# Optimization experiments

Measured on AMD Instinct MI355X. Metric: run time of the kernel, lower is better.

The kernel has to match this reference:

```python
import jax, jax.numpy as jnp
import numpy as np

D = 768

def _linear_params(key, name_idx, d_in, d_out):
    k1, k2 = jax.random.split(jax.random.fold_in(jax.random.key(42), name_idx))
    bound = 1.0 / np.sqrt(d_in)
    W = jax.random.uniform(k1, (d_out, d_in), jnp.float32, -bound, bound)
    b = jax.random.uniform(k2, (d_out,), jnp.float32, -bound, bound)
    return W, b

def setup_inputs() -> dict:
    key = jax.random.key(0)
    kq, kk, kv = jax.random.split(key, 3)
    B, S = 8, 2048
    inp = {
        'query': jax.random.normal(kq, (B, S, D), jnp.float32),
        'key': jax.random.normal(kk, (B, S, D), jnp.float32),
        'value': jax.random.normal(kv, (B, S, D), jnp.float32),
    }
    Wq, bq = _linear_params(key, 0, D, D)
    Wk, bk = _linear_params(key, 1, D, D)
    Wv, bv = _linear_params(key, 2, D, D)
    Wg1, bg1 = _linear_params(key, 3, D, D)
    Wg2, bg2 = _linear_params(key, 4, D, D)
    inp.update(Wq=Wq, bq=bq, Wk=Wk, bk=bk, Wv=Wv, bv=bv,
               Wg1=Wg1, bg1=bg1, Wg2=Wg2, bg2=bg2,
               text_scale=jnp.ones((1, D), jnp.float32))
    return inp

def reference(query, key, value, Wq, bq, Wk, bk, Wv, bv, Wg1, bg1, Wg2, bg2, text_scale):
    # Linear projections (torch Linear: x @ W.T + b)
    q = jnp.einsum('bsd,ed->bse', query, Wq) + bq
    k = jnp.einsum('bsd,ed->bse', key, Wk) + bk
    v = jnp.einsum('bsd,ed->bse', value, Wv) + bv
    scale = 1.0 / jnp.sqrt(jnp.float32(k.shape[-1]))
    scores = jnp.einsum('bqd,bkd->bqk', q, k) * scale  # [B, S, S]
    attn = jax.nn.softmax(scores, axis=-1)
    attended = jnp.einsum('bqk,bkd->bqd', attn, v)  # dropout = identity (eval)
    # text_gate: Linear -> ReLU -> Linear -> Sigmoid, then sigmoid applied AGAIN (faithful)
    h = jax.nn.relu(jnp.einsum('bsd,ed->bse', attended, Wg1) + bg1)
    gate = jax.nn.sigmoid(jnp.einsum('bsd,ed->bse', h, Wg2) + bg2)
    gated = jax.nn.sigmoid(gate) * attended * text_scale
    return gated
```

## Files before the change

kernel.cpp:

```cpp
#include <hip/hip_runtime.h>

typedef unsigned short ushort_t;
typedef __bf16 bf16x8 __attribute__((ext_vector_type(8)));
typedef float f32x4 __attribute__((ext_vector_type(4)));
typedef short short8 __attribute__((ext_vector_type(8)));

#define SBAR()   asm volatile("s_barrier" ::: "memory")
#define WAITV0() asm volatile("s_waitcnt vmcnt(0)" ::: "memory")
#define WAITV4() asm volatile("s_waitcnt vmcnt(4)" ::: "memory")

__device__ __forceinline__ float bf2f(unsigned short u) {
    union { unsigned int i; float f; } v; v.i = ((unsigned int)u) << 16; return v.f;
}
__device__ __forceinline__ unsigned short f2bf(float f) {
    union { float f; unsigned int i; } v; v.f = f;
    unsigned int r = v.i + 0x7fffu + ((v.i >> 16) & 1u);
    return (unsigned short)(r >> 16);
}
__device__ __forceinline__ float sigm(float x) { return 1.0f / (1.0f + __expf(-x)); }

__device__ __forceinline__ void async_copy16(const ushort_t* src, ushort_t* dst_lds) {
    __builtin_amdgcn_global_load_lds(
        (const __attribute__((address_space(1))) void*)src,
        (__attribute__((address_space(3))) void*)dst_lds,
        16, 0, 0);
}

#define WSEG 589824
#define NWALL 2949120
#define NTOT 2953728
__global__ __launch_bounds__(256)
void convert_params(const float* __restrict__ Wq, const float* __restrict__ Wk,
                    const float* __restrict__ Wv, const float* __restrict__ Wg1,
                    const float* __restrict__ Wg2, const float* __restrict__ bq,
                    const float* __restrict__ bk, const float* __restrict__ bv,
                    const float* __restrict__ bg1, const float* __restrict__ bg2,
                    const float* __restrict__ ts, ushort_t* __restrict__ dst)
{
    int i = (blockIdx.x * 256 + threadIdx.x) * 8;
    if (i >= NTOT) return;
    const float* src; int off;
    if (i < NWALL) {
        int wi = i / WSEG; off = i - wi * WSEG;
        src = (wi == 0) ? Wq : (wi == 1) ? Wk : (wi == 2) ? Wv : (wi == 3) ? Wg1 : Wg2;
    } else {
        int j = i - NWALL; int bi = j / 768; off = j - bi * 768;
        src = (bi == 0) ? bq : (bi == 1) ? bk : (bi == 2) ? bv : (bi == 3) ? bg1 : (bi == 4) ? bg2 : ts;
    }
    float4 a = *(const float4*)(src + off);
    float4 b = *(const float4*)(src + off + 4);
    short8 o;
    o[0] = (short)f2bf(a.x); o[1] = (short)f2bf(a.y); o[2] = (short)f2bf(a.z); o[3] = (short)f2bf(a.w);
    o[4] = (short)f2bf(b.x); o[5] = (short)f2bf(b.y); o[6] = (short)f2bf(b.z); o[7] = (short)f2bf(b.w);
    *(short8*)(dst + i) = o;
}

#define PERT 12582912ll
__global__ __launch_bounds__(256)
void convert_inputs(const float* __restrict__ q, const float* __restrict__ k,
                    const float* __restrict__ v, ushort_t* __restrict__ X)
{
    long long i = ((long long)blockIdx.x * 256 + threadIdx.x) * 8;
    const float* src; long long off;
    if (i < PERT)          { src = q; off = i; }
    else if (i < 2 * PERT) { src = k; off = i - PERT; }
    else                   { src = v; off = i - 2 * PERT; }
    float4 a = *(const float4*)(src + off);
    float4 b = *(const float4*)(src + off + 4);
    short8 o;
    o[0] = (short)f2bf(a.x); o[1] = (short)f2bf(a.y); o[2] = (short)f2bf(a.z); o[3] = (short)f2bf(a.w);
    o[4] = (short)f2bf(b.x); o[5] = (short)f2bf(b.y); o[6] = (short)f2bf(b.z); o[7] = (short)f2bf(b.w);
    *(short8*)(X + i) = o;
}

__global__ __launch_bounds__(256)
void rowsum_inv(const ushort_t* __restrict__ P, float* __restrict__ rinv, int S)
{
    const size_t row = blockIdx.x;
    const ushort_t* p = P + row * (size_t)S;
    const int tid = threadIdx.x;
    const int lane = tid & 63, wave = tid >> 6;

    short8 raw = *(const short8*)(p + tid * 8);
    float s = 0.f;
    #pragma unroll
    for (int j = 0; j < 8; ++j) s += bf2f((unsigned short)raw[j]);
    #pragma unroll
    for (int o = 32; o > 0; o >>= 1) s += __shfl_xor(s, o);
    __shared__ float red[4];
    if (lane == 0) red[wave] = s;
    __syncthreads();
    if (tid == 0) rinv[row] = 1.0f / (red[0] + red[1] + red[2] + red[3]);
}

template<int EPI, int CF32, int QKV>
__global__ __launch_bounds__(256, 2)
void gemm_bt(const ushort_t* __restrict__ A, const ushort_t* __restrict__ B,
             void* __restrict__ Cv, void* __restrict__ Cv2,
             const ushort_t* __restrict__ bias,
             const ushort_t* __restrict__ aux, const ushort_t* __restrict__ ts,
             const float* __restrict__ rinvg,
             int M, int N, int K, float scale,
             long long batchA, long long batchB, long long batchC)
{
    __shared__ __align__(16) ushort_t As[2][128 * 32];
    __shared__ __align__(16) ushort_t Bs[2][128 * 32];
    const int tid  = threadIdx.x;
    const int lane = tid & 63;
    const int wave = tid >> 6;
    const int wr = wave >> 1, wc = wave & 1;

    const int gx = gridDim.x, gy = gridDim.y;
    const int nwg = gx * gy * gridDim.z;
    int fid = (blockIdx.z * gy + blockIdx.y) * gx + blockIdx.x;
    fid = (fid & 7) * (nwg >> 3) + (fid >> 3);
    const int bz  = fid / (gx * gy);
    const int rem = fid - bz * (gx * gy);
    const int by  = rem / gx;
    const int bx  = rem - by * gx;
    const int row0 = by * 128;
    const int col0 = bx * 128;

    f32x4 acc[4][4] = {};

    const int srow = tid >> 2;
    const int scol = (tid & 3) * 8;
    const ushort_t* ga0 = A + batchA * bz + (size_t)(row0 + srow) * K + scol;
    const ushort_t* gb0 = B + batchB * bz + (size_t)(col0 + srow) * K + scol;

    const int kop  = (lane >> 4) * 8;
    const int arow = wr * 64 + (lane & 15);
    const int brow = wc * 64 + (lane & 15);

    const int NT = K >> 5;

    async_copy16(ga0,                  As[0] + tid * 8);
    async_copy16(ga0 + (size_t)64 * K, As[0] + 2048 + tid * 8);
    async_copy16(gb0,                  Bs[0] + tid * 8);
    async_copy16(gb0 + (size_t)64 * K, Bs[0] + 2048 + tid * 8);

    for (int t = 0; t < NT; ++t) {
        const int cur = t & 1;
        if (t + 1 < NT) {
            const int k1 = (t + 1) * 32;
            async_copy16(ga0 + k1,                  As[cur ^ 1] + tid * 8);
            async_copy16(ga0 + (size_t)64 * K + k1, As[cur ^ 1] + 2048 + tid * 8);
            async_copy16(gb0 + k1,                  Bs[cur ^ 1] + tid * 8);
            async_copy16(gb0 + (size_t)64 * K + k1, Bs[cur ^ 1] + 2048 + tid * 8);
            WAITV4();
        } else {
            WAITV0();
        }
        SBAR();
        bf16x8 af[4], bfr[4];
        #pragma unroll
        for (int m = 0; m < 4; ++m)
            af[m] = *(const bf16x8*)(As[cur] + (arow + m * 16) * 32 + kop);
        #pragma unroll
        for (int n = 0; n < 4; ++n)
            bfr[n] = *(const bf16x8*)(Bs[cur] + (brow + n * 16) * 32 + kop);
        #pragma unroll
        for (int m = 0; m < 4; ++m)
            #pragma unroll
            for (int n = 0; n < 4; ++n)
                acc[m][n] = __builtin_amdgcn_mfma_f32_16x16x32_bf16(af[m], bfr[n], acc[m][n], 0, 0, 0);
        SBAR();
    }

    const int r0 = row0 + wr * 64 + (lane >> 4) * 4;
    const int c0 = col0 + wc * 64 + (lane & 15);

    float rv[4][4];
    if (EPI == 7) {
        #pragma unroll
        for (int m = 0; m < 4; ++m)
            #pragma unroll
            for (int r = 0; r < 4; ++r)
                rv[m][r] = rinvg[(size_t)bz * M + r0 + m * 16 + r];
    }

    ushort_t* Cb = (QKV && bz == 2) ? (ushort_t*)Cv2 : (ushort_t*)Cv + batchC * bz;
    float* Cf = (float*)Cv;
    #pragma unroll
    for (int m = 0; m < 4; ++m) {
        #pragma unroll
        for (int n = 0; n < 4; ++n) {
            const int col = c0 + n * 16;
            #pragma unroll
            for (int r = 0; r < 4; ++r) {
                const int row = r0 + m * 16 + r;
                float val = acc[m][n][r];
                if (EPI == 1) {
                    val += bf2f(bias[(QKV ? bz * 768 : 0) + col]);
                } else if (EPI == 3) {
                    val += bf2f(bias[col]);
                    val = fmaxf(val, 0.0f);
                } else if (EPI == 4) {
                    val += bf2f(bias[col]);
                    float g  = sigm(val);
                    float gg = sigm(g);
                    val = gg * bf2f(aux[(size_t)row * N + col]) * bf2f(ts[col]);
                } else if (EPI == 5) {
                    val = __expf(val * scale);
                } else if (EPI == 7) {
                    val *= rv[m][r];
                }
                if (CF32) Cf[(size_t)row * N + col] = val;
                else      Cb[(size_t)row * N + col] = f2bf(val);
            }
        }
    }
}

__global__ __launch_bounds__(256)
void transpose2d(const ushort_t* __restrict__ V, ushort_t* __restrict__ VT, int R, int Ccols)
{
    __shared__ ushort_t t[32][33];
    const size_t zoff = (size_t)blockIdx.z * R * Ccols;
    const int tx = threadIdx.x, ty = threadIdx.y;
    const int c = blockIdx.x * 32 + tx;
    const int rbase = blockIdx.y * 32;
    #pragma unroll
    for (int i = 0; i < 4; ++i)
        t[ty + i * 8][tx] = V[zoff + (size_t)(rbase + ty + i * 8) * Ccols + c];
    __syncthreads();
    const int r = rbase + tx;
    const int cbase = blockIdx.x * 32;
    #pragma unroll
    for (int i = 0; i < 4; ++i)
        VT[zoff + (size_t)(cbase + ty + i * 8) * R + r] = t[tx][ty + i * 8];
}

extern "C" void kernel_launch(void* const* d_in, const int* in_sizes, int n_in,
                              void* d_out, int out_size, void* d_ws, size_t ws_size,
                              hipStream_t stream)
{
    (void)in_sizes; (void)n_in; (void)out_size; (void)ws_size;
    const float* query = (const float*)d_in[0];
    const float* key_  = (const float*)d_in[1];
    const float* value = (const float*)d_in[2];
    const float* Wq  = (const float*)d_in[3];
    const float* bq  = (const float*)d_in[4];
    const float* Wk  = (const float*)d_in[5];
    const float* bk  = (const float*)d_in[6];
    const float* Wv  = (const float*)d_in[7];
    const float* bv  = (const float*)d_in[8];
    const float* Wg1 = (const float*)d_in[9];
    const float* bg1 = (const float*)d_in[10];
    const float* Wg2 = (const float*)d_in[11];
    const float* bg2 = (const float*)d_in[12];
    const float* tsc = (const float*)d_in[13];

    const int S = 2048, D = 768, Bc = 8;
    const int MS = Bc * S;
    const long long SD = (long long)S * D;
    const long long SS = (long long)S * S;
    const long long MSD = (long long)MS * D;

    char* ws = (char*)d_ws;
    ushort_t* q    = (ushort_t*)(ws);
    ushort_t* att  = q;
    ushort_t* k    = (ushort_t*)(ws + 25165824ll);
    float*    rinv = (float*)(ws + 25165824ll);
    ushort_t* h    = k;
    ushort_t* vT   = (ushort_t*)(ws + 50331648ll);
    ushort_t* X    = (ushort_t*)(ws + 50331648ll);
    ushort_t* P    = (ushort_t*)(ws + 75497472ll);
    ushort_t* Wb   = (ushort_t*)(ws + 142606336ll);
    ushort_t* v    = (ushort_t*)d_out;

    const int WQ = 0, WG1 = 1769472, WG2 = 2359296;
    const int BQ = 2949120, BG1 = 2951424, BG2 = 2952192, TSO = 2952960;

    const dim3 blk(256);
    const float scale = 0.03608439182435161f;

    convert_params<<<dim3((NTOT / 8 + 255) / 256), blk, 0, stream>>>(
        Wq, Wk, Wv, Wg1, Wg2, bq, bk, bv, bg1, bg2, tsc, Wb);
    convert_inputs<<<dim3(18432), blk, 0, stream>>>(query, key_, value, X);
    gemm_bt<1, 0, 1><<<dim3(D / 128, MS / 128, 3), blk, 0, stream>>>(
        X, Wb + WQ, q, v, Wb + BQ, nullptr, nullptr, nullptr,
        MS, D, D, 1.f, MSD, (long long)WSEG, MSD);
    transpose2d<<<dim3(D / 32, S / 32, Bc), dim3(32, 8), 0, stream>>>(v, vT, S, D);
    gemm_bt<5, 0, 0><<<dim3(S / 128, S / 128, Bc), blk, 0, stream>>>(
        q, k, P, nullptr, nullptr, nullptr, nullptr, nullptr,
        S, S, D, scale, SD, SD, SS);
    rowsum_inv<<<dim3(MS), blk, 0, stream>>>(P, rinv, S);
    gemm_bt<7, 0, 0><<<dim3(D / 128, S / 128, Bc), blk, 0, stream>>>(
        P, vT, att, nullptr, nullptr, nullptr, nullptr, rinv,
        S, D, S, 1.f, SS, SD, SD);
    gemm_bt<3, 0, 0><<<dim3(D / 128, MS / 128, 1), blk, 0, stream>>>(
        att, Wb + WG1, h, nullptr, Wb + BG1, nullptr, nullptr, nullptr,
        MS, D, D, 1.f, 0, 0, 0);
    gemm_bt<4, 1, 0><<<dim3(D / 128, MS / 128, 1), blk, 0, stream>>>(
        h, Wb + WG2, d_out, nullptr, Wb + BG2, att, Wb + TSO, nullptr,
        MS, D, D, 1.f, 0, 0, 0);
}
```

Measured before the change: 337.3 us.

## Fuse softmax row sums into exp GEMM epilogue and triple-buffer LDS pipeline

The QK^T exp GEMM now reduces each 128x128 tile's row sums in registers and shared memory and writes per-tile partial sums. A tiny finalize kernel combines them into reciprocals, replacing a kernel that re-read the full bf16 probability matrix. All GEMMs also move from double to triple buffering of LDS tiles, prefetching two k-steps ahead. This costs extra shared memory per block, which may affect occupancy, and sums unrounded fp32 exps instead of bf16 values.

```diff
diff --git a/kernel.cpp b/kernel.cpp
--- a/kernel.cpp
+++ b/kernel.cpp
@@ -8,6 +8,7 @@
 #define SBAR()   asm volatile("s_barrier" ::: "memory")
 #define WAITV0() asm volatile("s_waitcnt vmcnt(0)" ::: "memory")
 #define WAITV4() asm volatile("s_waitcnt vmcnt(4)" ::: "memory")
+#define WAITV8() asm volatile("s_waitcnt vmcnt(8)" ::: "memory")
 
 __device__ __forceinline__ float bf2f(unsigned short u) {
     union { unsigned int i; float f; } v; v.i = ((unsigned int)u) << 16; return v.f;
@@ -74,23 +75,13 @@
 }
 
 __global__ __launch_bounds__(256)
-void rowsum_inv(const ushort_t* __restrict__ P, float* __restrict__ rinv, int S)
-{
-    const size_t row = blockIdx.x;
-    const ushort_t* p = P + row * (size_t)S;
-    const int tid = threadIdx.x;
-    const int lane = tid & 63, wave = tid >> 6;
-
-    short8 raw = *(const short8*)(p + tid * 8);
+void finalize_rinv(const float* __restrict__ psums, float* __restrict__ rinv, int nb)
+{
+    int row = blockIdx.x * 256 + threadIdx.x;
+    const float* p = psums + (size_t)row * nb;
     float s = 0.f;
-    #pragma unroll
-    for (int j = 0; j < 8; ++j) s += bf2f((unsigned short)raw[j]);
-    #pragma unroll
-    for (int o = 32; o > 0; o >>= 1) s += __shfl_xor(s, o);
-    __shared__ float red[4];
-    if (lane == 0) red[wave] = s;
-    __syncthreads();
-    if (tid == 0) rinv[row] = 1.0f / (red[0] + red[1] + red[2] + red[3]);
+    for (int i = 0; i < nb; ++i) s += p[i];
+    rinv[row] = 1.0f / s;
 }
 
 template<int EPI, int CF32, int QKV>
@@ -99,12 +90,13 @@
              void* __restrict__ Cv, void* __restrict__ Cv2,
              const ushort_t* __restrict__ bias,
              const ushort_t* __restrict__ aux, const ushort_t* __restrict__ ts,
-             const float* __restrict__ rinvg,
+             const float* __restrict__ rinvg, float* __restrict__ psum_out,
              int M, int N, int K, float scale,
              long long batchA, long long batchB, long long batchC)
 {
-    __shared__ __align__(16) ushort_t As[2][128 * 32];
-    __shared__ __align__(16) ushort_t Bs[2][128 * 32];
+    __shared__ __align__(16) ushort_t As[3][128 * 32];
+    __shared__ __align__(16) ushort_t Bs[3][128 * 32];
+    __shared__ float rsmx[256];
     const int tid  = threadIdx.x;
     const int lane = tid & 63;
     const int wave = tid >> 6;
@@ -134,38 +126,46 @@
 
     const int NT = K >> 5;
 
-    async_copy16(ga0,                  As[0] + tid * 8);
-    async_copy16(ga0 + (size_t)64 * K, As[0] + 2048 + tid * 8);
-    async_copy16(gb0,                  Bs[0] + tid * 8);
-    async_copy16(gb0 + (size_t)64 * K, Bs[0] + 2048 + tid * 8);
-
+#define STAGE4(T, BUF) do { const int kk_ = (T) * 32; \
+    async_copy16(ga0 + kk_,                  &As[BUF][0] + tid * 8); \
+    async_copy16(ga0 + (size_t)64 * K + kk_, &As[BUF][0] + 2048 + tid * 8); \
+    async_copy16(gb0 + kk_,                  &Bs[BUF][0] + tid * 8); \
+    async_copy16(gb0 + (size_t)64 * K + kk_, &Bs[BUF][0] + 2048 + tid * 8); \
+} while (0)
+
+    STAGE4(0, 0);
+    STAGE4(1, 1);
+
+    int cur = 0;
     for (int t = 0; t < NT; ++t) {
-        const int cur = t & 1;
-        if (t + 1 < NT) {
-            const int k1 = (t + 1) * 32;
-            async_copy16(ga0 + k1,                  As[cur ^ 1] + tid * 8);
-            async_copy16(ga0 + (size_t)64 * K + k1, As[cur ^ 1] + 2048 + tid * 8);
-            async_copy16(gb0 + k1,                  Bs[cur ^ 1] + tid * 8);
-            async_copy16(gb0 + (size_t)64 * K + k1, Bs[cur ^ 1] + 2048 + tid * 8);
+        if (t + 2 < NT) {
+            int nb = cur + 2; if (nb >= 3) nb -= 3;
+            STAGE4(t + 2, nb);
+            WAITV8();
+        } else if (t + 1 < NT) {
             WAITV4();
         } else {
             WAITV0();
         }
         SBAR();
+        const ushort_t* Ac = &As[0][0] + cur * 4096;
+        const ushort_t* Bc = &Bs[0][0] + cur * 4096;
         bf16x8 af[4], bfr[4];
         #pragma unroll
         for (int m = 0; m < 4; ++m)
-            af[m] = *(const bf16x8*)(As[cur] + (arow + m * 16) * 32 + kop);
+            af[m] = *(const bf16x8*)(Ac + (arow + m * 16) * 32 + kop);
         #pragma unroll
         for (int n = 0; n < 4; ++n)
-            bfr[n] = *(const bf16x8*)(Bs[cur] + (brow + n * 16) * 32 + kop);
+            bfr[n] = *(const bf16x8*)(Bc + (brow + n * 16) * 32 + kop);
         #pragma unroll
         for (int m = 0; m < 4; ++m)
             #pragma unroll
             for (int n = 0; n < 4; ++n)
                 acc[m][n] = __builtin_amdgcn_mfma_f32_16x16x32_bf16(af[m], bfr[n], acc[m][n], 0, 0, 0);
         SBAR();
-    }
+        ++cur; if (cur >= 3) cur = 0;
+    }
+#undef STAGE4
 
     const int r0 = row0 + wr * 64 + (lane >> 4) * 4;
     const int c0 = col0 + wc * 64 + (lane & 15);
@@ -178,6 +178,7 @@
             for (int r = 0; r < 4; ++r)
                 rv[m][r] = rinvg[(size_t)bz * M + r0 + m * 16 + r];
     }
+    float rsum[4][4] = {};
 
     ushort_t* Cb = (QKV && bz == 2) ? (ushort_t*)Cv2 : (ushort_t*)Cv + batchC * bz;
     float* Cf = (float*)Cv;
@@ -202,12 +203,40 @@
                     val = gg * bf2f(aux[(size_t)row * N + col]) * bf2f(ts[col]);
                 } else if (EPI == 5) {
                     val = __expf(val * scale);
+                    rsum[m][r] += val;
                 } else if (EPI == 7) {
                     val *= rv[m][r];
                 }
                 if (CF32) Cf[(size_t)row * N + col] = val;
                 else      Cb[(size_t)row * N + col] = f2bf(val);
             }
+        }
+    }
+
+    if (EPI == 5) {
+        #pragma unroll
+        for (int m = 0; m < 4; ++m)
+            #pragma unroll
+            for (int r = 0; r < 4; ++r) {
+                float s = rsum[m][r];
+                s += __shfl_xor(s, 1);
+                s += __shfl_xor(s, 2);
+                s += __shfl_xor(s, 4);
+                s += __shfl_xor(s, 8);
+                rsum[m][r] = s;
+            }
+        if ((lane & 15) == 0) {
+            const int quad = lane >> 4;
+            #pragma unroll
+            for (int m = 0; m < 4; ++m)
+                #pragma unroll
+                for (int r = 0; r < 4; ++r)
+                    rsmx[(wr * 64 + m * 16 + quad * 4 + r) * 2 + wc] = rsum[m][r];
+        }
+        __syncthreads();
+        if (tid < 128) {
+            float s = rsmx[tid * 2] + rsmx[tid * 2 + 1];
+            psum_out[((size_t)bz * M + row0 + tid) * gx + bx] = s;
         }
     }
 }
@@ -268,6 +297,7 @@
     ushort_t* P    = (ushort_t*)(ws + 75497472ll);
     ushort_t* Wb   = (ushort_t*)(ws + 142606336ll);
     ushort_t* v    = (ushort_t*)d_out;
+    float*  psums  = (float*)d_out;
 
     const int WQ = 0, WG1 = 1769472, WG2 = 2359296;
     const int BQ = 2949120, BG1 = 2951424, BG2 = 2952192, TSO = 2952960;
@@ -279,20 +309,20 @@
         Wq, Wk, Wv, Wg1, Wg2, bq, bk, bv, bg1, bg2, tsc, Wb);
     convert_inputs<<<dim3(18432), blk, 0, stream>>>(query, key_, value, X);
     gemm_bt<1, 0, 1><<<dim3(D / 128, MS / 128, 3), blk, 0, stream>>>(
-        X, Wb + WQ, q, v, Wb + BQ, nullptr, nullptr, nullptr,
+        X, Wb + WQ, q, v, Wb + BQ, nullptr, nullptr, nullptr, nullptr,
         MS, D, D, 1.f, MSD, (long long)WSEG, MSD);
     transpose2d<<<dim3(D / 32, S / 32, Bc), dim3(32, 8), 0, stream>>>(v, vT, S, D);
     gemm_bt<5, 0, 0><<<dim3(S / 128, S / 128, Bc), blk, 0, stream>>>(
-        q, k, P, nullptr, nullptr, nullptr, nullptr, nullptr,
+        q, k, P, nullptr, nullptr, nullptr, nullptr, nullptr, psums,
         S, S, D, scale, SD, SD, SS);
-    rowsum_inv<<<dim3(MS), blk, 0, stream>>>(P, rinv, S);
+    finalize_rinv<<<dim3(MS / 256), blk, 0, stream>>>(psums, rinv, S / 128);
     gemm_bt<7, 0, 0><<<dim3(D / 128, S / 128, Bc), blk, 0, stream>>>(
-        P, vT, att, nullptr, nullptr, nullptr, nullptr, rinv,
+        P, vT, att, nullptr, nullptr, nullptr, nullptr, rinv, nullptr,
         S, D, S, 1.f, SS, SD, SD);
     gemm_bt<3, 0, 0><<<dim3(D / 128, MS / 128, 1), blk, 0, stream>>>(
-        att, Wb + WG1, h, nullptr, Wb + BG1, nullptr, nullptr, nullptr,
+        att, Wb + WG1, h, nullptr, Wb + BG1, nullptr, nullptr, nullptr, nullptr,
         MS, D, D, 1.f, 0, 0, 0);
     gemm_bt<4, 1, 0><<<dim3(D / 128, MS / 128, 1), blk, 0, stream>>>(
-        h, Wb + WG2, d_out, nullptr, Wb + BG2, att, Wb + TSO, nullptr,
+        h, Wb + WG2, d_out, nullptr, Wb + BG2, att, Wb + TSO, nullptr, nullptr,
         MS, D, D, 1.f, 0, 0, 0);
 }
```

New measurement: 332.3 us. No clear change (-1.5%).
